# Optimization experiments

Measured on AMD Instinct MI355X. Metric: run time of the kernel, lower is better.

The kernel has to match this reference:

```python
import jax, jax.numpy as jnp
from jax import lax
import numpy as np

B = 16384
D = 32
N_HEADS = 4


def _piece_table():
    base = np.zeros((7, 4, 4), np.int32)
    cells = [
        [(1, 0), (1, 1), (1, 2), (1, 3)],  # I
        [(1, 1), (1, 2), (2, 1), (2, 2)],  # O
        [(1, 1), (2, 0), (2, 1), (2, 2)],  # T
        [(1, 1), (1, 2), (2, 0), (2, 1)],  # S
        [(1, 0), (1, 1), (2, 1), (2, 2)],  # Z
        [(1, 0), (2, 0), (2, 1), (2, 2)],  # J
        [(1, 2), (2, 0), (2, 1), (2, 2)],  # L
    ]
    for i, cs in enumerate(cells):
        for (r, c) in cs:
            base[i, r, c] = 1
    rots = np.stack([np.stack([np.rot90(base[i], k) for k in range(4)]) for i in range(7)])
    p = np.concatenate([rots, np.zeros((1, 4, 4, 4), np.int32)], 0)  # [8,4,4,4]
    return jnp.asarray(p)


def setup_inputs() -> dict:
    key = jax.random.key(0)
    ks = jax.random.split(key, 24)

    def ri(k, n, lo, hi):
        return jax.random.randint(k, (B, n), lo, hi, dtype=jnp.int32)

    t = jnp.concatenate([
        ri(ks[0], 1, 0, 10),   # col0 feature
        ri(ks[1], 1, 2, 8),
        ri(ks[2], 1, 0, 10),   # col2 y pos
        ri(ks[3], 1, 0, 8),    # col3 drop dist
        ri(ks[4], 1, 0, 4),    # col4 rotation
        ri(ks[5], 3, 0, 10),   # cols5-7
        ri(ks[6], 1, 0, 7),    # col8 piece id
        ri(ks[7], 6, 0, 7),    # cols9-14 hold/next
        ri(ks[8], 7, 0, 10),   # cols15-21
        ri(ks[9], 210, 0, 2),  # cols22-231 board
    ], axis=1)

    s = 0.05
    rn = lambda k, shp: jax.random.normal(k, shp, jnp.float32) * s
    return {
        "t": t,
        "piece_table": _piece_table(),
        "conv1_w": rn(ks[10], (6, 3, 5, 5)), "conv1_b": rn(ks[11], (6,)),
        "conv2_w": rn(ks[12], (16, 6, 5, 5)), "conv2_b": rn(ks[13], (16,)),
        "conv3_w": rn(ks[14], (64, 16, 3, 1)), "conv3_b": rn(ks[15], (64,)),
        "lfc1_w": rn(ks[16], (32, 64)), "lfc1_b": rn(ks[17], (32,)),
        "fc_w": rn(ks[18], (32, 8)), "fc_b": rn(ks[19], (32,)),
        "emb": rn(ks[20], (8, D)),
        "in_proj_w": rn(ks[21], (3 * D, D)), "in_proj_b": jnp.zeros((3 * D,), jnp.float32),
        "out_proj_w": rn(ks[22], (D, D)), "out_proj_b": jnp.zeros((D,), jnp.float32),
    }


def _avgpool2(x):
    b, c, h, w = x.shape
    h2, w2 = h // 2, w // 2
    return x[:, :, :h2 * 2, :w2 * 2].reshape(b, c, h2, 2, w2, 2).mean((3, 5))


def _lenet(x, w1, b1, w2, b2, w3, b3, fw, fb):
    dn = ("NCHW", "OIHW", "NCHW")
    x = jax.nn.relu(lax.conv_general_dilated(x, w1, (1, 1), ((2, 2), (2, 2)), dimension_numbers=dn) + b1[None, :, None, None])
    x = _avgpool2(x)                                   # [B,6,11,6]
    x = jax.nn.relu(lax.conv_general_dilated(x, w2, (1, 1), ((0, 0), (0, 0)), dimension_numbers=dn) + b2[None, :, None, None])
    x = _avgpool2(x)                                   # [B,16,3,1]
    x = jax.nn.relu(lax.conv_general_dilated(x, w3, (1, 1), ((0, 0), (0, 0)), dimension_numbers=dn) + b3[None, :, None, None])
    x = x.reshape(-1, 64)
    return jax.nn.relu(x @ fw.T + fb)                  # [B,32]


def _pe():
    pos = jnp.array([0, 0, 1, 2, 3, 4, 5], jnp.float32)[:, None]
    div = jnp.exp(jnp.arange(0, D, 2, dtype=jnp.float32) * (-jnp.log(10000.0) / D))
    s, c = jnp.sin(pos * div), jnp.cos(pos * div)      # [7,16] each
    return jnp.stack([s, c], -1).reshape(7, D)         # interleaved sin/cos


def _mha(q_in, kv, in_w, in_b, out_w, out_b):
    qw, kw, vw = in_w[:D], in_w[D:2 * D], in_w[2 * D:]
    qb, kb, vb = in_b[:D], in_b[D:2 * D], in_b[2 * D:]
    b, lq, _ = q_in.shape
    hd = D // N_HEADS
    q = (q_in @ qw.T + qb).reshape(b, lq, N_HEADS, hd)
    k = (kv @ kw.T + kb).reshape(b, -1, N_HEADS, hd)
    v = (kv @ vw.T + vb).reshape(b, -1, N_HEADS, hd)
    scores = jnp.einsum("bqhd,bkhd->bhqk", q, k) / jnp.sqrt(jnp.float32(hd))
    w = jax.nn.softmax(scores, axis=-1)
    o = jnp.einsum("bhqk,bkhd->bqhd", w, v).reshape(b, lq, D)
    return o @ out_w.T + out_b


def reference(t, piece_table, conv1_w, conv1_b, conv2_w, conv2_b, conv3_w, conv3_b,
              lfc1_w, lfc1_b, fc_w, fc_b, emb, in_proj_w, in_proj_b, out_proj_w, out_proj_b):
    bsz = t.shape[0]
    board = jnp.zeros((bsz, 3, 21, 10), jnp.float32)
    board = board.at[:, 0].set(t[:, 22:232].astype(jnp.float32).reshape(bsz, 21, 10))

    # gather piece grid, extract the 4 filled cells per sample in row-major order
    pieces = piece_table[t[:, 8], t[:, 4]].reshape(bsz, 16)        # [B,16] in {0,1}
    idx = jnp.argsort(1 - pieces, axis=1, stable=True)[:, :4]      # first 4 ones, scan order
    cy, cx = idx // 4, idx % 4
    x = cx + t[:, 1][:, None] - 2
    y = cy + t[:, 2][:, None]
    ny = y + t[:, 3][:, None]
    mask = (y >= 0) & (ny >= 0)
    br = jnp.arange(bsz, dtype=jnp.int32)[:, None]
    y_m = jnp.where(mask, y, -1)
    ny_m = jnp.where(mask, ny, -1)
    board = board.at[br, 1, y_m, x].set(1.0, mode="drop")
    board = board.at[br, 2, ny_m, x].set(1.0, mode="drop")

    board = jnp.pad(board, ((0, 0), (0, 0), (0, 1), (1, 1)), constant_values=1.0)  # [B,3,22,12]

    t9 = jnp.where((t[:, 9] != -1) & (t[:, 6] != 0), t[:, 9], 7)
    hold_next = jnp.concatenate([t[:, 8:9], t9[:, None], t[:, 10:15]], axis=1)     # [B,7]

    b2 = _lenet(board, conv1_w, conv1_b, conv2_w, conv2_b, conv3_w, conv3_b, lfc1_w, lfc1_b)  # [B,32]
    bkv = b2[:, None, :]                                            # [B,1,32]
    p = emb[hold_next] + _pe()[None]                                # [B,7,32]
    a = _mha(p, bkv, in_proj_w, in_proj_b, out_proj_w, out_proj_b)  # [B,7,32]

    xf = jax.nn.relu(t[:, :8].astype(jnp.float32) @ fc_w.T + fc_b)  # [B,32]
    out = jnp.concatenate([xf, a.mean(axis=1), b2], axis=1)         # [B,96]
    return (out, board)
```

## Files before the change

kernel.cpp:

```cpp
#include <hip/hip_runtime.h>
#include <cstddef>


#define BATCH 16384
#define SPB   4
#define NBLK  (BATCH / SPB)
#define RS    18
#define SBE_SZ 432
#define P1OFF  432
#define PCSOFF 800
#define SS2    816

#define BSYNC() asm volatile("s_waitcnt lgkmcnt(0)\ns_barrier" ::: "memory")

static __device__ __forceinline__ float dot4(float4 a, float4 b) {
  return a.x * b.x + a.y * b.y + a.z * b.z + a.w * b.w;
}

__global__ __launch_bounds__(256)
void cborder_kernel(const float* __restrict__ w1, float* __restrict__ cb)
{
  int i = blockIdx.x * 256 + threadIdx.x;
  if (i >= 1584) return;
  int p = i / 6, o = i - p * 6;
  int y0 = p / 12, x0 = p - y0 * 12;
  float acc = 0.f;
#pragma unroll
  for (int dy = 0; dy < 5; ++dy)
#pragma unroll
    for (int dx = 0; dx < 5; ++dx) {
      int pr = y0 + dy - 2, pc = x0 + dx - 2;
      if (pr >= 0 && pr < 22 && pc >= 0 && pc < 12 &&
          (pr == 21 || pc == 0 || pc == 11)) {
        int k = dy * 5 + dx;
        acc += w1[(o * 3 + 0) * 25 + k] + w1[(o * 3 + 1) * 25 + k]
             + w1[(o * 3 + 2) * 25 + k];
      }
    }
  cb[p * 6 + o] = acc;
}

__global__ __launch_bounds__(256, 4)
void board_model_kernel(const int* __restrict__ t,
                        const int* __restrict__ piece_table,
                        const float* __restrict__ w1, const float* __restrict__ b1,
                        const float* __restrict__ w2, const float* __restrict__ b2w,
                        const float* __restrict__ w3, const float* __restrict__ b3,
                        const float* __restrict__ wf1, const float* __restrict__ bf1,
                        const float* __restrict__ fcw, const float* __restrict__ fcb,
                        const float* __restrict__ ipw, const float* __restrict__ ipb,
                        const float* __restrict__ opw, const float* __restrict__ opb,
                        const float* __restrict__ cbg,
                        float* __restrict__ out,
                        float* __restrict__ out_board)
{
  __shared__ __align__(16) float scr[SPB * SS2];
  __shared__ float w1L[300];
  __shared__ float cbL[1440];

  const int tid  = threadIdx.x;
  const int lane = tid & 63;
  const int wv   = tid >> 6;
  const int bb   = blockIdx.x * SPB;

  for (int i = tid; i < 300; i += 256) {
    int o = i % 6, tt = i / 6, m = tt / 25, tp = tt - m * 25;
    w1L[i] = w1[(o * 3 + m + 1) * 25 + tp];
  }
  for (int i = tid; i < 1440; i += 256) cbL[i] = cbg[i];

  {
    float* W = &scr[wv * SS2];
    int*   pcs = (int*)&scr[wv * SS2 + PCSOFF];
    int*   bmi = (int*)&scr[wv * SS2 + P1OFF];
    const int* tr = t + (size_t)(bb + wv) * 232;

    float4* W4 = (float4*)W;
    for (int i = lane; i < 108; i += 64) W4[i] = float4{0.f, 0.f, 0.f, 0.f};
    if (lane < 44) bmi[lane] = 0;

    {
      const int2* cp = (const int2*)(tr + 22);
      for (int v = lane; v < 105; v += 64) {
        int2 cv = cp[v];
        int i0 = v * 2;
        int r = i0 / 10, b = i0 - r * 10;
        W[(r + 2) * RS + b + 5] = (float)cv.x;
        W[(r + 2) * RS + b + 6] = (float)cv.y;
      }
    }

    {
      const int* pt = piece_table + (tr[8] * 4 + tr[4]) * 16;
      int ptv = (lane < 16) ? pt[lane] : 0;
      unsigned long long bal = __ballot(ptv != 0);
      if (lane < 4) {
        unsigned x = (unsigned)bal & 0xffffu;
        for (int k = 0; k < lane; ++k) x &= x - 1;
        int sel = __builtin_ctz(x);
        int cy = sel >> 2, cx = sel & 3;
        int xx = cx + tr[1] - 2;
        int y  = cy + tr[2];
        int ny = y + tr[3];
        bool mask = (y >= 0) && (ny >= 0);
        bool xok  = (xx >= 0) && (xx < 10);
        bool v1 = mask && xok && (y < 21);
        bool v2 = mask && xok && (ny < 21);
        pcs[2 * lane + 0]       = v1 ? y  : -100;
        pcs[2 * lane + 1]       = xx + 1;
        pcs[2 * (lane + 4)]     = v2 ? ny : -100;
        pcs[2 * (lane + 4) + 1] = xx + 1;
        if (v1) atomicOr(&bmi[y],       1 << (xx + 1));
        if (v2) atomicOr(&bmi[22 + ny], 1 << (xx + 1));
      }
    }
    __builtin_amdgcn_wave_barrier();

    float* ob = out_board + (size_t)(bb + wv) * 792;
    for (int v = lane; v < 198; v += 64) {
      int ch = v / 66, w = v - ch * 66;
      int r = w / 3, c = (w - r * 3) * 4;
      float val[4];
      if (ch == 0) {
#pragma unroll
        for (int d = 0; d < 4; ++d) {
          int cd = c + d;
          val[d] = (r == 21 || cd == 0 || cd == 11) ? 1.f
                 : W[(r + 2) * RS + cd + 4];
        }
      } else {
        int bits = bmi[(ch - 1) * 22 + r];
#pragma unroll
        for (int d = 0; d < 4; ++d) {
          int cd = c + d;
          val[d] = (r == 21 || cd == 0 || cd == 11 || ((bits >> cd) & 1)) ? 1.f : 0.f;
        }
      }
      *(float4*)(ob + v * 4) = float4{val[0], val[1], val[2], val[3]};
    }
  }
  BSYNC();

  if (lane < 60) {
    int p = lane;
    int r = p / 6, c = p - r * 6;
    const float* Wq  = &scr[wv * SS2];
    const int*   pcs = (const int*)&scr[wv * SS2 + PCSOFF];

    int prA[8], pcA[8];
#pragma unroll
    for (int e = 0; e < 8; ++e) { prA[e] = pcs[2 * e]; pcA[e] = pcs[2 * e + 1]; }

    float rw[6][6];
    {
      const float* base = Wq + (2 * r) * RS + (2 * c + 2);
#pragma unroll
      for (int u = 0; u < 6; ++u) {
        float2 a0 = *(const float2*)(base + u * RS);
        float2 a1 = *(const float2*)(base + u * RS + 2);
        float2 a2 = *(const float2*)(base + u * RS + 4);
        rw[u][0] = a0.x; rw[u][1] = a0.y; rw[u][2] = a1.x;
        rw[u][3] = a1.y; rw[u][4] = a2.x; rw[u][5] = a2.y;
      }
    }

    float acc[2][2][6];
#pragma unroll
    for (int i = 0; i < 2; ++i)
#pragma unroll
      for (int j = 0; j < 2; ++j) {
        int pcell = (2 * r + i) * 12 + (2 * c + j);
#pragma unroll
        for (int o = 0; o < 6; ++o)
          acc[i][j][o] = b1[o] + cbL[pcell * 6 + o];
      }

#pragma unroll
    for (int u = 0; u < 6; ++u) {
#pragma unroll
      for (int i = 0; i < 2; ++i) {
        if (u - i < 0 || u - i > 4) continue;
        const int ky = u - i;
#pragma unroll
        for (int j = 0; j < 2; ++j)
#pragma unroll
          for (int kx = 0; kx < 5; ++kx) {
            float xv = rw[u][j + kx];
#pragma unroll
            for (int o = 0; o < 6; ++o)
              acc[i][j][o] += xv * w1[o * 75 + ky * 5 + kx];
          }
      }
    }

#pragma unroll
    for (int e = 0; e < 8; ++e) {
      int pr = prA[e];
      if (pr < 0) continue;
      int pc = pcA[e];
      int chm = e >> 2;
      int dyb = pr + 2 - 2 * r;
      int dxb = pc + 2 - 2 * c;
      if (dyb < 0 || dyb > 5 || dxb < 0 || dxb > 5) continue;
#pragma unroll
      for (int i = 0; i < 2; ++i) {
        int dy = dyb - i;
        if ((unsigned)dy >= 5u) continue;
#pragma unroll
        for (int j = 0; j < 2; ++j) {
          int dx = dxb - j;
          if ((unsigned)dx >= 5u) continue;
          const float* wp = &w1L[(chm * 25 + dy * 5 + dx) * 6];
#pragma unroll
          for (int o = 0; o < 6; ++o)
            acc[i][j][o] += wp[o];
        }
      }
    }

    float* P1q = &scr[wv * SS2 + P1OFF];
#pragma unroll
    for (int o = 0; o < 6; ++o) {
      float v = fmaxf(acc[0][0][o], 0.f) + fmaxf(acc[0][1][o], 0.f)
              + fmaxf(acc[1][0][o], 0.f) + fmaxf(acc[1][1][o], 0.f);
      P1q[o * 61 + p] = 0.25f * v;
    }
  }
  BSYNC();

  const int wvu = __builtin_amdgcn_readfirstlane(wv);

  if (lane < 48) {
    int q = lane / 12, p = lane - q * 12;
    int r = p >> 1, c = p & 1;
    const float* P1q = &scr[q * SS2 + P1OFF];
    float a4[4];
#pragma unroll
    for (int oo = 0; oo < 4; ++oo) a4[oo] = b2w[4 * wvu + oo];
#pragma unroll
    for (int ic = 0; ic < 6; ++ic) {
      float vals[29];
      const float* pb = P1q + ic * 61 + r * 6 + c;
#pragma unroll
      for (int m = 0; m < 29; ++m) vals[m] = pb[m];
#pragma unroll
      for (int kr = 0; kr < 5; ++kr)
#pragma unroll
        for (int kc = 0; kc < 5; ++kc) {
          float xv = vals[kr * 6 + kc];
#pragma unroll
          for (int oo = 0; oo < 4; ++oo)
            a4[oo] += xv * w2[(((4 * wvu + oo) * 6 + ic) * 5 + kr) * 5 + kc];
        }
    }
    float* C2q = &scr[q * SS2];
#pragma unroll
    for (int oo = 0; oo < 4; ++oo)
      C2q[(4 * wvu + oo) * 12 + p] = fmaxf(a4[oo], 0.f);
  }
  BSYNC();

  {
    const int q = wvu;
    float* S = &scr[q * SS2];

    if (lane < 48) {
      int o = lane / 3, pr = lane - o * 3;
      float4 v4 = *(const float4*)(S + o * 12 + 4 * pr);
      S[192 + lane] = 0.25f * (v4.x + v4.y + v4.z + v4.w);
    }
    __builtin_amdgcn_wave_barrier();

    {
      int o = lane;
      const float4* w34 = (const float4*)(w3 + o * 48);
      const float4* S4  = (const float4*)(S + 192);
      float acc = b3[o];
#pragma unroll
      for (int m = 0; m < 12; ++m)
        acc += dot4(S4[m], w34[m]);
      S[240 + o] = fmaxf(acc, 0.f);
    }
    __builtin_amdgcn_wave_barrier();

    {
      int j = lane & 31, h = lane >> 5;
      const float4* wf4 = (const float4*)(wf1 + j * 64 + 32 * h);
      const float4* S4  = (const float4*)(S + 240 + 32 * h);
      float part = 0.f;
#pragma unroll
      for (int m = 0; m < 8; ++m)
        part += dot4(S4[m], wf4[m]);
      part += __shfl_xor(part, 32, 64);
      if (h == 0) {
        float acc = fmaxf(bf1[j] + part, 0.f);
        S[304 + j] = acc;
        out[(size_t)(bb + q) * 96 + 64 + j] = acc;
      }
    }
    __builtin_amdgcn_wave_barrier();

    {
      int j = lane & 31;
      if (lane < 32) {
        const float4* ip4 = (const float4*)(ipw + (size_t)(64 + j) * 32);
        const float4* S4  = (const float4*)(S + 304);
        float acc = ipb[64 + j];
#pragma unroll
        for (int m = 0; m < 8; ++m)
          acc += dot4(S4[m], ip4[m]);
        S[336 + j] = acc;
      } else {
        const int4* t4 = (const int4*)(t + (size_t)(bb + q) * 232);
        int4 ta = t4[0], tb = t4[1];
        const float4* fc4 = (const float4*)(fcw + j * 8);
        float4 wa = fc4[0], wb = fc4[1];
        float acc = fcb[j]
                  + (float)ta.x * wa.x + (float)ta.y * wa.y
                  + (float)ta.z * wa.z + (float)ta.w * wa.w
                  + (float)tb.x * wb.x + (float)tb.y * wb.y
                  + (float)tb.z * wb.z + (float)tb.w * wb.w;
        out[(size_t)(bb + q) * 96 + j] = fmaxf(acc, 0.f);
      }
    }
    __builtin_amdgcn_wave_barrier();

    if (lane < 32) {
      int j = lane;
      const float4* op4 = (const float4*)(opw + j * 32);
      const float4* S4  = (const float4*)(S + 336);
      float acc = opb[j];
#pragma unroll
      for (int m = 0; m < 8; ++m)
        acc += dot4(S4[m], op4[m]);
      out[(size_t)(bb + q) * 96 + 32 + j] = acc;
    }
  }
}

extern "C" void kernel_launch(void* const* d_in, const int* in_sizes, int n_in,
                              void* d_out, int out_size, void* d_ws, size_t ws_size,
                              hipStream_t stream) {
  const int*   t   = (const int*)d_in[0];
  const int*   pt  = (const int*)d_in[1];
  const float* w1  = (const float*)d_in[2];
  const float* b1  = (const float*)d_in[3];
  const float* w2  = (const float*)d_in[4];
  const float* b2w = (const float*)d_in[5];
  const float* w3  = (const float*)d_in[6];
  const float* b3  = (const float*)d_in[7];
  const float* wf1 = (const float*)d_in[8];
  const float* bf1 = (const float*)d_in[9];
  const float* fcw = (const float*)d_in[10];
  const float* fcb = (const float*)d_in[11];
  const float* ipw = (const float*)d_in[13];
  const float* ipb = (const float*)d_in[14];
  const float* opw = (const float*)d_in[15];
  const float* opb = (const float*)d_in[16];

  float* out       = (float*)d_out;
  float* out_board = out + (size_t)BATCH * 96;
  float* cbg       = (float*)d_ws;

  hipLaunchKernelGGL(cborder_kernel, dim3(7), dim3(256), 0, stream, w1, cbg);
  hipLaunchKernelGGL(board_model_kernel, dim3(NBLK), dim3(256), 0, stream,
                     t, pt, w1, b1, w2, b2w, w3, b3, wf1, bf1, fcw, fcb,
                     ipw, ipb, opw, opb, cbg, out, out_board);
}
```

Measured before the change: 193.8 us.

## Store pooled conv1 pixel-major for vector LDS loads; pass piece cells via shuffle

Pooled conv1 activations are now stored interleaved as 8 floats per pixel, reusing the board scratch area. This lets conv2 fetch its 5x5x6 window with float4 LDS reads instead of many scalar reads. The per-piece cell coordinates are packed into one register and broadcast with wave shuffles instead of going through shared memory. Shared-memory offsets are reorganized to match. The price is a slightly larger per-sample scratch and more register pressure in conv2 from holding 10 float4s.

```diff
diff --git a/kernel.cpp b/kernel.cpp
--- a/kernel.cpp
+++ b/kernel.cpp
@@ -6,12 +6,17 @@
 #define SPB   4
 #define NBLK  (BATCH / SPB)
 #define RS    18
-#define SBE_SZ 432
-#define P1OFF  432
-#define PCSOFF 800
-#define SS2    816
+#define SS2    824
+#define C2OFF  480
+#define P2OFF  672
+#define C3OFF  720
+#define B2OFF  784
+#define VOFF   720
 
 #define BSYNC() asm volatile("s_waitcnt lgkmcnt(0)\ns_barrier" ::: "memory")
+
+#define AF(A, i) ((i & 3) == 0 ? A[(i) >> 2].x : (i & 3) == 1 ? A[(i) >> 2].y \
+                : (i & 3) == 2 ? A[(i) >> 2].z : A[(i) >> 2].w)
 
 static __device__ __forceinline__ float dot4(float4 a, float4 b) {
   return a.x * b.x + a.y * b.y + a.z * b.z + a.w * b.w;
@@ -69,10 +74,11 @@
   }
   for (int i = tid; i < 1440; i += 256) cbL[i] = cbg[i];
 
+  int packed = 0;
+
   {
     float* W = &scr[wv * SS2];
-    int*   pcs = (int*)&scr[wv * SS2 + PCSOFF];
-    int*   bmi = (int*)&scr[wv * SS2 + P1OFF];
+    int*   bmi = (int*)&scr[wv * SS2 + C2OFF];
     const int* tr = t + (size_t)(bb + wv) * 232;
 
     float4* W4 = (float4*)W;
@@ -106,10 +112,8 @@
         bool xok  = (xx >= 0) && (xx < 10);
         bool v1 = mask && xok && (y < 21);
         bool v2 = mask && xok && (ny < 21);
-        pcs[2 * lane + 0]       = v1 ? y  : -100;
-        pcs[2 * lane + 1]       = xx + 1;
-        pcs[2 * (lane + 4)]     = v2 ? ny : -100;
-        pcs[2 * (lane + 4) + 1] = xx + 1;
+        packed = (v1 ? (y & 31) : 31) | ((v2 ? (ny & 31) : 31) << 5)
+               | (((xx + 2) & 15) << 10);
         if (v1) atomicOr(&bmi[y],       1 << (xx + 1));
         if (v2) atomicOr(&bmi[22 + ny], 1 << (xx + 1));
       }
@@ -141,15 +145,21 @@
   }
   BSYNC();
 
+  int prA[8], pcA[8];
+#pragma unroll
+  for (int e = 0; e < 4; ++e) {
+    int pk = __shfl(packed, e, 64);
+    int r1 = pk & 31, r2 = (pk >> 5) & 31, pcc = ((pk >> 10) & 15) - 1;
+    prA[e]     = (r1 == 31) ? -100 : r1;
+    pcA[e]     = pcc;
+    prA[e + 4] = (r2 == 31) ? -100 : r2;
+    pcA[e + 4] = pcc;
+  }
+
   if (lane < 60) {
     int p = lane;
     int r = p / 6, c = p - r * 6;
-    const float* Wq  = &scr[wv * SS2];
-    const int*   pcs = (const int*)&scr[wv * SS2 + PCSOFF];
-
-    int prA[8], pcA[8];
-#pragma unroll
-    for (int e = 0; e < 8; ++e) { prA[e] = pcs[2 * e]; pcA[e] = pcs[2 * e + 1]; }
+    float* Wq = &scr[wv * SS2];
 
     float rw[6][6];
     {
@@ -218,13 +228,13 @@
       }
     }
 
-    float* P1q = &scr[wv * SS2 + P1OFF];
-#pragma unroll
-    for (int o = 0; o < 6; ++o) {
-      float v = fmaxf(acc[0][0][o], 0.f) + fmaxf(acc[0][1][o], 0.f)
-              + fmaxf(acc[1][0][o], 0.f) + fmaxf(acc[1][1][o], 0.f);
-      P1q[o * 61 + p] = 0.25f * v;
-    }
+    float v[6];
+#pragma unroll
+    for (int o = 0; o < 6; ++o)
+      v[o] = 0.25f * (fmaxf(acc[0][0][o], 0.f) + fmaxf(acc[0][1][o], 0.f)
+                    + fmaxf(acc[1][0][o], 0.f) + fmaxf(acc[1][1][o], 0.f));
+    *(float4*)(Wq + p * 8)     = float4{v[0], v[1], v[2], v[3]};
+    *(float2*)(Wq + p * 8 + 4) = float2{v[4], v[5]};
   }
   BSYNC();
 
@@ -233,27 +243,28 @@
   if (lane < 48) {
     int q = lane / 12, p = lane - q * 12;
     int r = p >> 1, c = p & 1;
-    const float* P1q = &scr[q * SS2 + P1OFF];
+    const float* P1q = &scr[q * SS2];
     float a4[4];
 #pragma unroll
     for (int oo = 0; oo < 4; ++oo) a4[oo] = b2w[4 * wvu + oo];
 #pragma unroll
-    for (int ic = 0; ic < 6; ++ic) {
-      float vals[29];
-      const float* pb = P1q + ic * 61 + r * 6 + c;
-#pragma unroll
-      for (int m = 0; m < 29; ++m) vals[m] = pb[m];
-#pragma unroll
-      for (int kr = 0; kr < 5; ++kr)
-#pragma unroll
-        for (int kc = 0; kc < 5; ++kc) {
-          float xv = vals[kr * 6 + kc];
+    for (int kr = 0; kr < 5; ++kr) {
+      const float4* pp = (const float4*)(P1q + ((r + kr) * 6 + c) * 8);
+      float4 A[10];
+#pragma unroll
+      for (int m = 0; m < 10; ++m) A[m] = pp[m];
+#pragma unroll
+      for (int kc = 0; kc < 5; ++kc)
+#pragma unroll
+        for (int ic = 0; ic < 6; ++ic) {
+          const int idx = kc * 8 + ic;
+          float xv = AF(A, idx);
 #pragma unroll
           for (int oo = 0; oo < 4; ++oo)
             a4[oo] += xv * w2[(((4 * wvu + oo) * 6 + ic) * 5 + kr) * 5 + kc];
         }
     }
-    float* C2q = &scr[q * SS2];
+    float* C2q = &scr[q * SS2 + C2OFF];
 #pragma unroll
     for (int oo = 0; oo < 4; ++oo)
       C2q[(4 * wvu + oo) * 12 + p] = fmaxf(a4[oo], 0.f);
@@ -266,27 +277,27 @@
 
     if (lane < 48) {
       int o = lane / 3, pr = lane - o * 3;
-      float4 v4 = *(const float4*)(S + o * 12 + 4 * pr);
-      S[192 + lane] = 0.25f * (v4.x + v4.y + v4.z + v4.w);
+      float4 v4 = *(const float4*)(S + C2OFF + o * 12 + 4 * pr);
+      S[P2OFF + lane] = 0.25f * (v4.x + v4.y + v4.z + v4.w);
     }
     __builtin_amdgcn_wave_barrier();
 
     {
       int o = lane;
       const float4* w34 = (const float4*)(w3 + o * 48);
-      const float4* S4  = (const float4*)(S + 192);
+      const float4* S4  = (const float4*)(S + P2OFF);
       float acc = b3[o];
 #pragma unroll
       for (int m = 0; m < 12; ++m)
         acc += dot4(S4[m], w34[m]);
-      S[240 + o] = fmaxf(acc, 0.f);
+      S[C3OFF + o] = fmaxf(acc, 0.f);
     }
     __builtin_amdgcn_wave_barrier();
 
     {
       int j = lane & 31, h = lane >> 5;
       const float4* wf4 = (const float4*)(wf1 + j * 64 + 32 * h);
-      const float4* S4  = (const float4*)(S + 240 + 32 * h);
+      const float4* S4  = (const float4*)(S + C3OFF + 32 * h);
       float part = 0.f;
 #pragma unroll
       for (int m = 0; m < 8; ++m)
@@ -294,7 +305,7 @@
       part += __shfl_xor(part, 32, 64);
       if (h == 0) {
         float acc = fmaxf(bf1[j] + part, 0.f);
-        S[304 + j] = acc;
+        S[B2OFF + j] = acc;
         out[(size_t)(bb + q) * 96 + 64 + j] = acc;
       }
     }
@@ -304,12 +315,12 @@
       int j = lane & 31;
       if (lane < 32) {
         const float4* ip4 = (const float4*)(ipw + (size_t)(64 + j) * 32);
-        const float4* S4  = (const float4*)(S + 304);
+        const float4* S4  = (const float4*)(S + B2OFF);
         float acc = ipb[64 + j];
 #pragma unroll
         for (int m = 0; m < 8; ++m)
           acc += dot4(S4[m], ip4[m]);
-        S[336 + j] = acc;
+        S[VOFF + j] = acc;
       } else {
         const int4* t4 = (const int4*)(t + (size_t)(bb + q) * 232);
         int4 ta = t4[0], tb = t4[1];
@@ -328,7 +339,7 @@
     if (lane < 32) {
       int j = lane;
       const float4* op4 = (const float4*)(opw + j * 32);
-      const float4* S4  = (const float4*)(S + 336);
+      const float4* S4  = (const float4*)(S + VOFF);
       float acc = opb[j];
 #pragma unroll
       for (int m = 0; m < 8; ++m)
```

After: 321.1 us. 1.66x slower.

## Make each wave process its own sample end-to-end, replacing block barriers

Applied to the files above, without the earlier changes.

Conv2 is reassigned so each wave computes all 16 output channels for its own sample, rather than splitting output channels across waves. This lets the three block-wide barriers become wave barriers. A prep kernel now also writes a transposed copy of the conv2 weights, which each wave loads into shared memory for float4 reads. The border-correction table is padded to 8 per cell and read from global memory instead of LDS. The cost is redundant per-wave LDS fills, more LDS in use, and the occupancy hint dropped from the launch bounds.

```diff
diff --git a/kernel.cpp b/kernel.cpp
--- a/kernel.cpp
+++ b/kernel.cpp
@@ -6,41 +6,50 @@
 #define SPB   4
 #define NBLK  (BATCH / SPB)
 #define RS    18
-#define SBE_SZ 432
 #define P1OFF  432
 #define PCSOFF 800
 #define SS2    816
 
-#define BSYNC() asm volatile("s_waitcnt lgkmcnt(0)\ns_barrier" ::: "memory")
+#define WS_CB   0
+#define WS_W2T  2112
+#define WS_TOT  4512
 
 static __device__ __forceinline__ float dot4(float4 a, float4 b) {
   return a.x * b.x + a.y * b.y + a.z * b.z + a.w * b.w;
 }
 
 __global__ __launch_bounds__(256)
-void cborder_kernel(const float* __restrict__ w1, float* __restrict__ cb)
+void prep_kernel(const float* __restrict__ w1, const float* __restrict__ w2,
+                 float* __restrict__ ws)
 {
   int i = blockIdx.x * 256 + threadIdx.x;
-  if (i >= 1584) return;
-  int p = i / 6, o = i - p * 6;
-  int y0 = p / 12, x0 = p - y0 * 12;
-  float acc = 0.f;
-#pragma unroll
-  for (int dy = 0; dy < 5; ++dy)
-#pragma unroll
-    for (int dx = 0; dx < 5; ++dx) {
-      int pr = y0 + dy - 2, pc = x0 + dx - 2;
-      if (pr >= 0 && pr < 22 && pc >= 0 && pc < 12 &&
-          (pr == 21 || pc == 0 || pc == 11)) {
-        int k = dy * 5 + dx;
-        acc += w1[(o * 3 + 0) * 25 + k] + w1[(o * 3 + 1) * 25 + k]
-             + w1[(o * 3 + 2) * 25 + k];
-      }
-    }
-  cb[p * 6 + o] = acc;
+  if (i < 2112) {
+    int p = i >> 3, o = i & 7;
+    float acc = 0.f;
+    if (o < 6) {
+      int y0 = p / 12, x0 = p - y0 * 12;
+#pragma unroll
+      for (int dy = 0; dy < 5; ++dy)
+#pragma unroll
+        for (int dx = 0; dx < 5; ++dx) {
+          int pr = y0 + dy - 2, pc = x0 + dx - 2;
+          if (pr >= 0 && pr < 22 && pc >= 0 && pc < 12 &&
+              (pr == 21 || pc == 0 || pc == 11)) {
+            int k = dy * 5 + dx;
+            acc += w1[(o * 3 + 0) * 25 + k] + w1[(o * 3 + 1) * 25 + k]
+                 + w1[(o * 3 + 2) * 25 + k];
+          }
+        }
+    }
+    ws[WS_CB + i] = acc;
+  } else if (i < WS_TOT) {
+    int idx = i - WS_W2T;
+    int tap = idx >> 4, o = idx & 15;
+    ws[WS_W2T + idx] = w2[o * 150 + tap];
+  }
 }
 
-__global__ __launch_bounds__(256, 4)
+__global__ __launch_bounds__(256)
 void board_model_kernel(const int* __restrict__ t,
                         const int* __restrict__ piece_table,
                         const float* __restrict__ w1, const float* __restrict__ b1,
@@ -55,19 +64,23 @@
                         float* __restrict__ out_board)
 {
   __shared__ __align__(16) float scr[SPB * SS2];
-  __shared__ float w1L[300];
-  __shared__ float cbL[1440];
+  __shared__ __align__(16) float w1L[300];
+  __shared__ __align__(16) float w2L[2400];
 
   const int tid  = threadIdx.x;
   const int lane = tid & 63;
   const int wv   = tid >> 6;
   const int bb   = blockIdx.x * SPB;
 
-  for (int i = tid; i < 300; i += 256) {
+  for (int i = lane; i < 300; i += 64) {
     int o = i % 6, tt = i / 6, m = tt / 25, tp = tt - m * 25;
     w1L[i] = w1[(o * 3 + m + 1) * 25 + tp];
   }
-  for (int i = tid; i < 1440; i += 256) cbL[i] = cbg[i];
+  {
+    const float4* src = (const float4*)(cbg + WS_W2T);
+    float4* dst = (float4*)w2L;
+    for (int i = lane; i < 600; i += 64) dst[i] = src[i];
+  }
 
   {
     float* W = &scr[wv * SS2];
@@ -139,7 +152,9 @@
       *(float4*)(ob + v * 4) = float4{val[0], val[1], val[2], val[3]};
     }
   }
-  BSYNC();
+  __builtin_amdgcn_wave_barrier();
+
+  const int wvu = __builtin_amdgcn_readfirstlane(wv);
 
   if (lane < 60) {
     int p = lane;
@@ -165,14 +180,17 @@
     }
 
     float acc[2][2][6];
+    const float* cbp = cbg + WS_CB;
 #pragma unroll
     for (int i = 0; i < 2; ++i)
 #pragma unroll
       for (int j = 0; j < 2; ++j) {
         int pcell = (2 * r + i) * 12 + (2 * c + j);
-#pragma unroll
-        for (int o = 0; o < 6; ++o)
-          acc[i][j][o] = b1[o] + cbL[pcell * 6 + o];
+        float4 ca  = *(const float4*)(cbp + pcell * 8);
+        float2 ca2 = *(const float2*)(cbp + pcell * 8 + 4);
+        acc[i][j][0] = b1[0] + ca.x;  acc[i][j][1] = b1[1] + ca.y;
+        acc[i][j][2] = b1[2] + ca.z;  acc[i][j][3] = b1[3] + ca.w;
+        acc[i][j][4] = b1[4] + ca2.x; acc[i][j][5] = b1[5] + ca2.y;
       }
 
 #pragma unroll
@@ -226,17 +244,14 @@
       P1q[o * 61 + p] = 0.25f * v;
     }
   }
-  BSYNC();
-
-  const int wvu = __builtin_amdgcn_readfirstlane(wv);
+  __builtin_amdgcn_wave_barrier();
 
   if (lane < 48) {
-    int q = lane / 12, p = lane - q * 12;
+    int og = lane / 12, p = lane - og * 12;
     int r = p >> 1, c = p & 1;
-    const float* P1q = &scr[q * SS2 + P1OFF];
-    float a4[4];
-#pragma unroll
-    for (int oo = 0; oo < 4; ++oo) a4[oo] = b2w[4 * wvu + oo];
+    const float* P1q = &scr[wv * SS2 + P1OFF];
+    float4 bw = *(const float4*)(b2w + 4 * og);
+    float a0 = bw.x, a1 = bw.y, a2 = bw.z, a3 = bw.w;
 #pragma unroll
     for (int ic = 0; ic < 6; ++ic) {
       float vals[29];
@@ -247,18 +262,18 @@
       for (int kr = 0; kr < 5; ++kr)
 #pragma unroll
         for (int kc = 0; kc < 5; ++kc) {
+          float4 wt = *(const float4*)(&w2L[(ic * 25 + kr * 5 + kc) * 16 + 4 * og]);
           float xv = vals[kr * 6 + kc];
-#pragma unroll
-          for (int oo = 0; oo < 4; ++oo)
-            a4[oo] += xv * w2[(((4 * wvu + oo) * 6 + ic) * 5 + kr) * 5 + kc];
-        }
-    }
-    float* C2q = &scr[q * SS2];
-#pragma unroll
-    for (int oo = 0; oo < 4; ++oo)
-      C2q[(4 * wvu + oo) * 12 + p] = fmaxf(a4[oo], 0.f);
-  }
-  BSYNC();
+          a0 += xv * wt.x; a1 += xv * wt.y; a2 += xv * wt.z; a3 += xv * wt.w;
+        }
+    }
+    float* C2q = &scr[wv * SS2];
+    C2q[(4 * og + 0) * 12 + p] = fmaxf(a0, 0.f);
+    C2q[(4 * og + 1) * 12 + p] = fmaxf(a1, 0.f);
+    C2q[(4 * og + 2) * 12 + p] = fmaxf(a2, 0.f);
+    C2q[(4 * og + 3) * 12 + p] = fmaxf(a3, 0.f);
+  }
+  __builtin_amdgcn_wave_barrier();
 
   {
     const int q = wvu;
@@ -362,7 +377,7 @@
   float* out_board = out + (size_t)BATCH * 96;
   float* cbg       = (float*)d_ws;
 
-  hipLaunchKernelGGL(cborder_kernel, dim3(7), dim3(256), 0, stream, w1, cbg);
+  hipLaunchKernelGGL(prep_kernel, dim3(18), dim3(256), 0, stream, w1, w2, cbg);
   hipLaunchKernelGGL(board_model_kernel, dim3(NBLK), dim3(256), 0, stream,
                      t, pt, w1, b1, w2, b2w, w3, b3, wf1, bf1, fcw, fcb,
                      ipw, ipb, opw, opb, cbg, out, out_board);
```

Measured after the change: 207.1 us. +6.9%, slower.
